# Kernel optimization log

Measured on AMD Instinct MI355X. Metric: run time of the kernel, lower is better.

## Reference

```python
import jax, jax.numpy as jnp
import numpy as np

BN_EPS = 1e-5

def conv1x1(x, w, b):
    # x: [N,C,T,V], w: [O,C], b: [O]
    return jnp.einsum('nctv,oc->notv', x, w) + b[None, :, None, None]

def conv9(x, w, b):
    # (9,1) temporal conv, padding (4,0). x: [N,C,T,V], w: [O,C,9], b: [O]
    out = jax.lax.conv_general_dilated(
        x, w[:, :, :, None], window_strides=(1, 1), padding=((4, 4), (0, 0)),
        dimension_numbers=('NCHW', 'OIHW', 'NCHW'))
    return out + b[None, :, None, None]

def attn_adj(f1, f2):
    # f1,f2: [N,inter,T,V] -> softmax over rows (axis -2) of [N,V,V]
    N, ic, T, V = f1.shape
    a1 = jnp.transpose(f1, (0, 3, 1, 2)).reshape(N, V, ic * T)  # permute(0,3,1,2).view
    a2 = f2.reshape(N, ic * T, V)
    scores = jnp.einsum('nvk,nkw->nvw', a1, a2) / (ic * T)
    return jax.nn.softmax(scores, axis=-2)


def setup_inputs() -> dict:
    key = jax.random.key(0)
    ks = jax.random.split(key, 16)
    N, C, T, V, S, IC = 16, 256, 64, 25, 3, 64
    s = lambda k, shape, sc=0.05: jax.random.normal(k, shape, dtype=jnp.float32) * sc
    return {
        'x': jax.random.normal(ks[0], (N, C, T, V), dtype=jnp.float32),
        'A': jax.random.uniform(ks[1], (S, V, V), dtype=jnp.float32),
        'PA': s(ks[2], (S, V, V), 1e-3),
        'wa': s(ks[3], (S, IC, C)), 'ba': jnp.zeros((S, IC), jnp.float32),
        'wb': s(ks[4], (S, IC, C)), 'bb': jnp.zeros((S, IC), jnp.float32),
        'wT1': s(ks[5], (S, IC, C, 9)), 'bT1': jnp.zeros((S, IC), jnp.float32),
        'wT2': s(ks[6], (S, IC, C, 9)), 'bT2': jnp.zeros((S, IC), jnp.float32),
        'wST11': s(ks[7], (S, IC, C, 9)), 'bST11': jnp.zeros((S, IC), jnp.float32),
        'wST12': s(ks[8], (S, IC, C, 9)), 'bST12': jnp.zeros((S, IC), jnp.float32),
        'wd': s(ks[9], (S, C, C)), 'bd': jnp.zeros((S, C), jnp.float32),
        'gamma': jnp.ones((C,), jnp.float32), 'beta': jnp.zeros((C,), jnp.float32),
        'bn_mean': jnp.zeros((C,), jnp.float32), 'bn_var': jnp.ones((C,), jnp.float32),
    }


def reference(x, A, PA, wa, ba, wb, bb, wT1, bT1, wT2, bT2,
              wST11, bST11, wST12, bST12, wd, bd, gamma, beta, bn_mean, bn_var):
    N, C, T, V = x.shape
    I = jnp.eye(V, dtype=x.dtype)
    # Chebyshev-like static graph transforms (computed once in __init__ in torch)
    A_ch4s = jax.nn.softmax((8 * A**4 - 4 * A**2 - 4 * A + I) / V, axis=-2)
    A_ch3 = 4 * A**2 - A - 2 * I
    A_all = A_ch3 + A_ch4s + PA  # [3,V,V]

    xf = x.reshape(N, C * T, V)
    y = 0.0
    for i in range(3):
        A1 = attn_adj(conv1x1(x, wa[i], ba[i]), conv1x1(x, wb[i], bb[i]))
        AT = attn_adj(conv9(x, wT1[i], bT1[i]), conv9(x, wT2[i], bT2[i]))
        # ModuleList append quirk: even i -> 1x1 conv (center tap), odd i -> (9,1) conv
        if i % 2 == 0:
            s1 = conv1x1(x, wST11[i, :, :, 4], bST11[i])
            s2 = conv1x1(x, wST12[i, :, :, 4], bST12[i])
        else:
            s1 = conv9(x, wST11[i], bST11[i])
            s2 = conv9(x, wST12[i], bST12[i])
        AST = attn_adj(s1, s2)
        Ai = A_all[i] + A1 + AT + AST  # [N,V,V]
        z = jnp.einsum('nkv,nvw->nkw', xf, Ai).reshape(N, C, T, V)
        y = y + conv1x1(z, wd[i], bd[i])

    yb = (y - bn_mean[None, :, None, None]) * (gamma[None, :, None, None]
         / jnp.sqrt(bn_var[None, :, None, None] + BN_EPS)) + beta[None, :, None, None]
    return jax.nn.relu(yb + x)  # down is identity (in_channels == out_channels)
```

## Files before the change

### kernel.cpp

```cpp
#include <hip/hip_runtime.h>
#include <hip/hip_bf16.h>

#define NN 16
#define CC 256
#define TT 64
#define VV 25
#define ICC 64
#define TV 1600
#define CTV 409600
#define NICTV 1638400

typedef __bf16 v8bf __attribute__((ext_vector_type(8)));
typedef __bf16 v4bf __attribute__((ext_vector_type(4)));
typedef float f32x16 __attribute__((ext_vector_type(16)));

struct ConvPairs {
  const __bf16* wA[5];
  const __bf16* wB[5];
  const float*  bA[5];
  const float*  bB[5];
};

__device__ __forceinline__ void gl_lds16(const __bf16* g, __bf16* l){
  __builtin_amdgcn_global_load_lds(
      (const __attribute__((address_space(1))) unsigned int*)g,
      (__attribute__((address_space(3))) unsigned int*)l, 16, 0, 0);
}

__global__ __launch_bounds__(256) void prep_k(
    const float* __restrict__ x, __bf16* __restrict__ xt,
    const float* __restrict__ wT1, const float* __restrict__ wT2,
    const float* __restrict__ wST11, const float* __restrict__ wST12,
    __bf16* __restrict__ wT1p, __bf16* __restrict__ wT2p,
    __bf16* __restrict__ wS1p, __bf16* __restrict__ wS2p,
    const float* __restrict__ wa, const float* __restrict__ wb,
    __bf16* __restrict__ wabp, __bf16* __restrict__ wScp,
    const float* __restrict__ wd, __bf16* __restrict__ wdb,
    const float* __restrict__ A, const float* __restrict__ PA,
    float* __restrict__ Aall, __bf16* __restrict__ zp){
  __shared__ __align__(16) float smf[64*65];
  __bf16* smb = (__bf16*)smf;
  int b = blockIdx.x;
  int tid = threadIdx.x;
  if (b < 64){
    int t = b >> 3, ch64 = (b >> 1) & 3, o2 = b & 1;
    const float* src; __bf16* dst;
    if (t < 3)      { src = wT1  + (size_t)t*147456;     dst = wT1p + (size_t)t*147456; }
    else if (t < 6) { src = wT2  + (size_t)(t-3)*147456; dst = wT2p + (size_t)(t-3)*147456; }
    else if (t == 6){ src = wST11 + 147456;              dst = wS1p; }
    else            { src = wST12 + 147456;              dst = wS2p; }
    const float* in = src + (size_t)(o2*32)*2304 + ch64*576;
    for (int i = tid; i < 32*576; i += 256){
      int row = i / 576, cc = i % 576;
      smb[i] = (__bf16)in[(size_t)row*2304 + cc];
    }
    __syncthreads();
    for (int i = tid; i < 18432; i += 256){
      int e = i & 7, l = (i >> 3) & 63, ks = (i >> 9) & 1;
      int r10 = i >> 10;
      int tap = r10 % 9, chh = r10 / 9;
      int ol = l & 31, hh = l >> 5;
      int cl = ks*16 + hh*8 + e;
      int c64 = chh*32 + cl;
      int ch8 = ch64*2 + chh;
      dst[(size_t)((((ch8*9 + tap)*2 + ks)*2 + o2)*512) + l*8 + e]
          = smb[ol*576 + c64*9 + tap];
    }
  } else if (b < 74){
    int u = b - 64;
    for (int it = 0; it < 8; ++it){
      int i = tid + it*256;
      int e = i & 7, l = (i >> 3) & 63, o2 = (i >> 9) & 1;
      int ks = (i >> 10) & 1, ch = i >> 11;
      int ol = l & 31, hh = l >> 5;
      int o = o2*32 + ol;
      int c = ch*32 + ks*16 + hh*8 + e;
      __bf16 v;
      if (u < 6){
        const float* w = (u < 3) ? (wa + (size_t)u*16384) : (wb + (size_t)(u-3)*16384);
        v = (__bf16)w[(size_t)o*256 + c];
      } else {
        int i9 = ((u == 6) || (u == 8)) ? 0 : 2;
        const float* w = ((u < 8) ? wST11 : wST12) + (size_t)i9*147456;
        v = (__bf16)w[((size_t)o*256 + c)*9 + 4];
      }
      __bf16* dst = (u < 6) ? (wabp + (size_t)u*16384) : (wScp + (size_t)(u-6)*16384);
      dst[i] = v;
    }
  } else if (b < 842){
    int i = (b-74)*256 + tid;
    if (i < 196608) wdb[i] = (__bf16)wd[i];
  } else if (b == 842){
    int t = tid;
    if (t < 75){
      int s = t / 25, w = t % 25;
      float a[25], m[25];
      float mx = -3.4e38f;
      for (int v = 0; v < 25; ++v){
        float av = A[(s*25 + v)*25 + w];
        a[v] = av;
        float d = (v == w) ? 1.f : 0.f;
        float mm = (8.f*av*av*av*av - 4.f*av*av - 4.f*av + d) * 0.04f;
        m[v] = mm;
        mx = fmaxf(mx, mm);
      }
      float sum = 0.f;
      for (int v = 0; v < 25; ++v){ float e = __expf(m[v]-mx); m[v] = e; sum += e; }
      float inv = 1.f/sum;
      for (int v = 0; v < 25; ++v){
        float av = a[v];
        float d = (v == w) ? 1.f : 0.f;
        Aall[(s*25+v)*25 + w] = m[v]*inv + 4.f*av*av - av - 2.f*d + PA[(s*25+v)*25+w];
      }
    } else if (t >= 128){
      zp[t-128] = (__bf16)0.f;
    }
  } else {
    int idx = b - 843;
    int p0 = (idx % 25)*64, c0 = ((idx/25) & 3)*64, n = idx/100;
    for (int i = tid; i < 4096; i += 256){
      int cc = i >> 6, pp = i & 63;
      smf[cc*65+pp] = x[(size_t)n*CTV + (size_t)(c0+cc)*TV + p0 + pp];
    }
    __syncthreads();
    for (int i = tid; i < 4096; i += 256){
      int pp = i >> 6, cc = i & 63;
      xt[((size_t)n*TV + p0+pp)*256 + c0+cc] = (__bf16)smf[cc*65+pp];
    }
  }
}

template<int NTAPS>
__global__ __launch_bounds__(512, 2) void conv11_k(const __bf16* __restrict__ xt,
    ConvPairs cp, const __bf16* __restrict__ zp, __bf16* __restrict__ fbuf){
  extern __shared__ __bf16 sm[];
  constexpr int HALO  = (NTAPS==9) ? 100 : 0;
  constexpr int NROWS = 512 + 2*HALO;
  constexpr int SLOTS = NROWS*4;
  constexpr int KSTG  = (SLOTS + 511)/512;
  constexpr int NSTEP = NTAPS*2;
  int p0 = blockIdx.x*512;
  int n  = blockIdx.y;
  int pr = blockIdx.z;
  int tid = threadIdx.x;
  int lane = tid & 63;
  int wave = tid >> 6;
  int which = wave >> 2, wq = wave & 3;
  int h = lane >> 5, l31 = lane & 31;
  const __bf16* wp = (which ? cp.wB[pr] : cp.wA[pr]) + lane*8;
  const __bf16* xtn = xt + (size_t)n*CTV;
  __bf16* buf0 = sm;
  __bf16* buf1 = sm + NROWS*32;

  f32x16 acc[2][4];
  #pragma unroll
  for (int a=0;a<2;++a)
    #pragma unroll
    for (int b=0;b<4;++b)
      #pragma unroll
      for (int r=0;r<16;++r) acc[a][b][r] = 0.f;

  int rowbase = wq*128 + l31;

  auto stage = [&](__bf16* bn, int ch){
    #pragma unroll
    for (int k=0; k<KSTG; ++k){
      int slot = k*512 + tid;
      if ((SLOTS & 511) && slot >= SLOTS) continue;
      int row = slot >> 2, g2 = slot & 3;
      int g = (g2 - row) & 3;
      int pg = p0 - HALO + row;
      const __bf16* src = ((unsigned)pg < 1600u)
          ? (xtn + (size_t)pg*256 + ch*32 + g*8) : (zp + g*8);
      gl_lds16(src, bn + (size_t)slot*8);
    }
  };
  auto ldA = [&](int ch, int s, v8bf* aa){
    int tap = s >> 1, ks = s & 1;
    size_t o = (size_t)(((ch*NTAPS + tap)*2 + ks)*2)*512;
    aa[0] = *(const v8bf*)(wp + o);
    aa[1] = *(const v8bf*)(wp + o + 512);
  };
  auto ldB = [&](const __bf16* bc, int s, v8bf* bb){
    int tap = s >> 1, ks = s & 1;
    int rowb = (NTAPS==9 ? tap*25 : 0) + rowbase;
    #pragma unroll
    for (int pq=0; pq<4; ++pq){
      int row = rowb + pq*32;
      int gs = ((ks*2 + h) + row) & 3;
      bb[pq] = *(const v8bf*)(bc + row*32 + gs*8);
    }
  };

  v8bf ar[2][2];
  ldA(0, 0, ar[0]);
  ldA(0, 1, ar[1]);
  stage(buf0, 0);
  __syncthreads();

  for (int ch=0; ch<8; ++ch){
    const __bf16* bc = (ch & 1) ? buf1 : buf0;
    __bf16*       bn = (ch & 1) ? buf0 : buf1;
    if (ch < 7) stage(bn, ch+1);
    v8bf bR[2][4];
    ldB(bc, 0, bR[0]);
    ldB(bc, 1, bR[1]);
    #pragma unroll
    for (int s=0; s<NSTEP; ++s){
      int c = s & 1;
      v8bf A0 = ar[c][0], A1 = ar[c][1];
      v8bf B0 = bR[c][0], B1 = bR[c][1], B2 = bR[c][2], B3 = bR[c][3];
      if (s+2 < NSTEP){
        ldB(bc, s+2, bR[c]);
        ldA(ch, s+2, ar[c]);
      } else if (ch < 7){
        ldA(ch+1, s+2-NSTEP, ar[c]);
      }
      acc[0][0] = __builtin_amdgcn_mfma_f32_32x32x16_bf16(A0, B0, acc[0][0], 0,0,0);
      acc[1][0] = __builtin_amdgcn_mfma_f32_32x32x16_bf16(A1, B0, acc[1][0], 0,0,0);
      acc[0][1] = __builtin_amdgcn_mfma_f32_32x32x16_bf16(A0, B1, acc[0][1], 0,0,0);
      acc[1][1] = __builtin_amdgcn_mfma_f32_32x32x16_bf16(A1, B1, acc[1][1], 0,0,0);
      acc[0][2] = __builtin_amdgcn_mfma_f32_32x32x16_bf16(A0, B2, acc[0][2], 0,0,0);
      acc[1][2] = __builtin_amdgcn_mfma_f32_32x32x16_bf16(A1, B2, acc[1][2], 0,0,0);
      acc[0][3] = __builtin_amdgcn_mfma_f32_32x32x16_bf16(A0, B3, acc[0][3], 0,0,0);
      acc[1][3] = __builtin_amdgcn_mfma_f32_32x32x16_bf16(A1, B3, acc[1][3], 0,0,0);
    }
    __syncthreads();
  }

  const float* bias = which ? cp.bB[pr] : cp.bA[pr];
  __bf16* outb = fbuf + (size_t)(pr*2 + which)*NICTV + (size_t)n*TV*64;
  #pragma unroll
  for (int pq=0; pq<4; ++pq){
    int p = p0 + wq*128 + pq*32 + l31;
    if (p >= 1600) continue;
    __bf16* orow = outb + (size_t)p*64;
    #pragma unroll
    for (int of=0; of<2; ++of){
      #pragma unroll
      for (int g=0; g<4; ++g){
        int og = of*32 + 8*g + 4*h;
        v4bf pk;
        #pragma unroll
        for (int j=0;j<4;++j) pk[j] = (__bf16)(acc[of][pq][4*g+j] + bias[og+j]);
        *(v4bf*)(orow + og) = pk;
      }
    }
  }
}

__global__ __launch_bounds__(256, 2) void ugemm5_k(const __bf16* __restrict__ xt,
    const __bf16* __restrict__ wdb, __bf16* __restrict__ ubuf){
  extern __shared__ __bf16 sm[];
  int p0 = blockIdx.x*128;
  int n  = blockIdx.y;
  int br = blockIdx.z;
  int tid = threadIdx.x;
  int lane = tid & 63;
  int os = tid >> 6;
  int h = lane >> 5, l31 = lane & 31;
  const __bf16* xtn = xt + (size_t)n*CTV;

  f32x16 acc[2][4];
  #pragma unroll
  for (int a=0;a<2;++a)
    #pragma unroll
    for (int b=0;b<4;++b)
      #pragma unroll
      for (int r=0;r<16;++r) acc[a][b][r] = 0.f;

  for (int s2 = tid; s2 < 128*32; s2 += 256){
    int row = s2 >> 5, g = s2 & 31;
    int pg = p0 + row;
    uint4 val = make_uint4(0u,0u,0u,0u);
    if (pg < 1600)
      val = *(const uint4*)(xtn + (size_t)pg*256 + g*8);
    int gs = (g + row) & 31;
    *(uint4*)(sm + row*256 + gs*8) = val;
  }
  __syncthreads();

  const __bf16* wl = wdb + ((size_t)br*256 + os*64 + l31)*256 + h*8;
  auto ldA = [&](int ks, v8bf& A0, v8bf& A1){
    A0 = *(const v8bf*)(wl + ks*16);
    A1 = *(const v8bf*)(wl + (size_t)32*256 + ks*16);
  };
  auto ldB = [&](int ks, v8bf* bb){
    #pragma unroll
    for (int pq=0; pq<4; ++pq){
      int row = pq*32 + l31;
      int gs = ((ks*2 + h) + row) & 31;
      bb[pq] = *(const v8bf*)(sm + row*256 + gs*8);
    }
  };
  v8bf a0[4], a1[4];
  ldA(0, a0[0], a1[0]);
  ldA(1, a0[1], a1[1]);
  ldA(2, a0[2], a1[2]);
  ldA(3, a0[3], a1[3]);
  v8bf bR[2][4];
  ldB(0, bR[0]);
  ldB(1, bR[1]);
  #pragma unroll
  for (int ks=0; ks<16; ++ks){
    int c2 = ks & 1, cur = ks & 3;
    v8bf B0 = bR[c2][0], B1 = bR[c2][1], B2 = bR[c2][2], B3 = bR[c2][3];
    v8bf A0 = a0[cur], A1 = a1[cur];
    if (ks+2 < 16) ldB(ks+2, bR[c2]);
    if (ks+4 < 16) ldA(ks+4, a0[cur], a1[cur]);
    acc[0][0] = __builtin_amdgcn_mfma_f32_32x32x16_bf16(A0, B0, acc[0][0], 0,0,0);
    acc[1][0] = __builtin_amdgcn_mfma_f32_32x32x16_bf16(A1, B0, acc[1][0], 0,0,0);
    acc[0][1] = __builtin_amdgcn_mfma_f32_32x32x16_bf16(A0, B1, acc[0][1], 0,0,0);
    acc[1][1] = __builtin_amdgcn_mfma_f32_32x32x16_bf16(A1, B1, acc[1][1], 0,0,0);
    acc[0][2] = __builtin_amdgcn_mfma_f32_32x32x16_bf16(A0, B2, acc[0][2], 0,0,0);
    acc[1][2] = __builtin_amdgcn_mfma_f32_32x32x16_bf16(A1, B2, acc[1][2], 0,0,0);
    acc[0][3] = __builtin_amdgcn_mfma_f32_32x32x16_bf16(A0, B3, acc[0][3], 0,0,0);
    acc[1][3] = __builtin_amdgcn_mfma_f32_32x32x16_bf16(A1, B3, acc[1][3], 0,0,0);
  }

  #pragma unroll
  for (int pq=0; pq<4; ++pq){
    int p = p0 + pq*32 + l31;
    if (p >= 1600) continue;
    __bf16* out = ubuf + ((size_t)(br*NN + n)*TV + p)*256;
    #pragma unroll
    for (int oq=0; oq<2; ++oq){
      #pragma unroll
      for (int g=0; g<4; ++g){
        int og = os*64 + oq*32 + 8*g + 4*h;
        v4bf pk;
        #pragma unroll
        for (int j=0;j<4;++j) pk[j] = (__bf16)acc[oq][pq][4*g+j];
        *(v4bf*)(out + og) = pk;
      }
    }
  }
}

__global__ __launch_bounds__(256) void scores_m_k(const __bf16* __restrict__ fbuf,
                                                  float* __restrict__ part, int pairbase){
  int n = blockIdx.y, pr = blockIdx.z;
  int tid = threadIdx.x;
  int lane = tid & 63;
  int wave = tid >> 6;
  int chunk = blockIdx.x*4 + wave;
  int h = lane >> 5, l31 = lane & 31;
  const __bf16* f1 = fbuf + (size_t)(pr*2)*NICTV   + (size_t)n*TV*64;
  const __bf16* f2 = fbuf + (size_t)(pr*2+1)*NICTV + (size_t)n*TV*64;
  int t0 = chunk*4;

  f32x16 acc;
  #pragma unroll
  for (int r=0;r<16;++r) acc[r] = 0.f;

  auto off = [&](int s)->size_t{
    int t = t0 + (s>>2), og = s&3;
    return ((size_t)(t*25 + l31))*64 + og*16 + h*8;
  };
  v8bf A[4], B[4];
  #pragma unroll
  for (int i=0; i<4; ++i){
    size_t o = off(i);
    A[i] = *(const v8bf*)(f1+o); B[i] = *(const v8bf*)(f2+o);
  }
  #pragma unroll
  for (int s=0; s<16; ++s){
    int cur = s & 3;
    v8bf Ac = A[cur], Bc = B[cur];
    if (s+4 < 16){
      size_t o2 = off(s+4);
      A[cur] = *(const v8bf*)(f1+o2);
      B[cur] = *(const v8bf*)(f2+o2);
    }
    acc = __builtin_amdgcn_mfma_f32_32x32x16_bf16(Ac, Bc, acc, 0,0,0);
  }

  size_t tile = (((size_t)(pairbase+pr)*NN + n)*16 + chunk);
  float* pt = part + tile*1024;
  #pragma unroll
  for (int r=0; r<16; ++r){
    int row = (r&3) + 8*(r>>2) + 4*h;
    pt[row*32 + l31] = acc[r];
  }
}

__global__ __launch_bounds__(64) void reduce_all_k(const float* __restrict__ part,
    const float* __restrict__ Aall, float* __restrict__ Ai3){
  const int pairbr[9] = {0,1,2,0,2, 0,1,2,1};
  int n = blockIdx.x, w = blockIdx.y;
  int lane = threadIdx.x;
  float accbr[3] = {0.f, 0.f, 0.f};
  for (int pr=0; pr<9; ++pr){
    float s = 0.f;
    if (lane < 25){
      const float* pp = part + (((size_t)pr*NN + n)*16)*1024 + lane*32 + w;
      #pragma unroll
      for (int ch=0; ch<16; ++ch) s += pp[(size_t)ch*1024];
    }
    s *= (1.f/4096.f);
    float mval = (lane<25) ? s : -3.4e38f;
    #pragma unroll
    for (int d=32; d>0; d>>=1) mval = fmaxf(mval, __shfl_xor(mval, d));
    float e = (lane<25) ? __expf(s - mval) : 0.f;
    float sum = e;
    #pragma unroll
    for (int d=32; d>0; d>>=1) sum += __shfl_xor(sum, d);
    accbr[pairbr[pr]] += e / sum;
  }
  if (lane < 25){
    #pragma unroll
    for (int br=0; br<3; ++br)
      Ai3[((size_t)br*NN + n)*625 + lane*25 + w] =
        Aall[br*625 + lane*25 + w] + accbr[br];
  }
}

__global__ __launch_bounds__(256) void yep_k(const float* __restrict__ x,
    const float* __restrict__ Ai3, const __bf16* __restrict__ ubuf,
    const float* __restrict__ bd, const float* __restrict__ gamma,
    const float* __restrict__ beta, const float* __restrict__ bnm,
    const float* __restrict__ bnv, float* __restrict__ out){
  __shared__ float ais[3][25*28];
  int t = blockIdx.x, n = blockIdx.y, o = threadIdx.x;
  for (int l=o; l<2100; l+=256){
    int br = l/700, r = l%700;
    int v = r/28, w = r%28;
    ais[br][v*28+w] = (w<25) ? Ai3[((size_t)br*NN + n)*625 + v*25 + w] : 0.f;
  }
  __syncthreads();
  float y[28];
  #pragma unroll
  for (int w=0;w<28;++w) y[w]=0.f;
  for (int br=0; br<3; ++br){
    const __bf16* up = ubuf + ((size_t)(br*NN + n)*TV + t*25)*256 + o;
    float uv[25];
    #pragma unroll
    for (int v=0;v<25;++v) uv[v] = (float)up[(size_t)v*256];
    const float* ab = ais[br];
    for (int v=0; v<25; ++v){
      float u = uv[v];
      #pragma unroll
      for (int j=0; j<7; ++j){
        float4 a4 = *(const float4*)(ab + v*28 + 4*j);
        y[4*j+0] = fmaf(u, a4.x, y[4*j+0]);
        y[4*j+1] = fmaf(u, a4.y, y[4*j+1]);
        y[4*j+2] = fmaf(u, a4.z, y[4*j+2]);
        y[4*j+3] = fmaf(u, a4.w, y[4*j+3]);
      }
    }
  }
  float bsum = bd[o] + bd[256+o] + bd[512+o];
  float sc = gamma[o] * rsqrtf(bnv[o] + 1e-5f);
  float m  = bnm[o], be = beta[o];
  const float* xr = x + (size_t)n*CTV + (size_t)o*TV + t*25;
  float* orow = out + (size_t)n*CTV + (size_t)o*TV + t*25;
  #pragma unroll
  for (int w=0; w<25; ++w)
    orow[w] = fmaxf((y[w] + bsum - m)*sc + be + xr[w], 0.f);
}

extern "C" void kernel_launch(void* const* d_in, const int* in_sizes, int n_in,
                              void* d_out, int out_size, void* d_ws, size_t ws_size,
                              hipStream_t stream) {
  const float* x     = (const float*)d_in[0];
  const float* A     = (const float*)d_in[1];
  const float* PA    = (const float*)d_in[2];
  const float* wa    = (const float*)d_in[3];
  const float* ba    = (const float*)d_in[4];
  const float* wb    = (const float*)d_in[5];
  const float* bb    = (const float*)d_in[6];
  const float* wT1   = (const float*)d_in[7];
  const float* bT1   = (const float*)d_in[8];
  const float* wT2   = (const float*)d_in[9];
  const float* bT2   = (const float*)d_in[10];
  const float* wST11 = (const float*)d_in[11];
  const float* bST11 = (const float*)d_in[12];
  const float* wST12 = (const float*)d_in[13];
  const float* bST12 = (const float*)d_in[14];
  const float* wd    = (const float*)d_in[15];
  const float* bd    = (const float*)d_in[16];
  const float* gamma = (const float*)d_in[17];
  const float* beta  = (const float*)d_in[18];
  const float* bnm   = (const float*)d_in[19];
  const float* bnv   = (const float*)d_in[20];

  char* W = (char*)d_ws;
  float*  Aall = (float*)W;  W += 8192;
  __bf16* zp   = (__bf16*)W; W += 256;
  float*  Ai3  = (float*)W;  W += 122880;
  __bf16* wabp = (__bf16*)W; W += 196608;
  __bf16* wScp = (__bf16*)W; W += 131072;
  __bf16* wT1p = (__bf16*)W; W += 884736;
  __bf16* wT2p = (__bf16*)W; W += 884736;
  __bf16* wS1p = (__bf16*)W; W += 294912;
  __bf16* wS2p = (__bf16*)W; W += 294912;
  __bf16* wdb  = (__bf16*)W; W += 393216;
  __bf16* xt   = (__bf16*)W; W += 13107200;
  char* R = W;               W += 39321600;
  float*  part = (float*)W;  W += 9437184;
  __bf16* fbuf = (__bf16*)R;
  __bf16* ubuf = (__bf16*)R;

  prep_k<<<2443, 256, 0, stream>>>(x, xt, wT1, wT2, wST11, wST12,
                                   wT1p, wT2p, wS1p, wS2p,
                                   wa, wb, wabp, wScp, wd, wdb, A, PA, Aall, zp);

  {
    ConvPairs cp;
    for (int i=0;i<3;++i){
      cp.wA[i] = wabp + (size_t)i*16384;      cp.wB[i] = wabp + (size_t)(3+i)*16384;
      cp.bA[i] = ba + i*64;                   cp.bB[i] = bb + i*64;
    }
    int evens[2] = {0, 2};
    for (int j=0;j<2;++j){
      int i = evens[j];
      cp.wA[3+j] = wScp + (size_t)j*16384;    cp.wB[3+j] = wScp + (size_t)(2+j)*16384;
      cp.bA[3+j] = bST11 + i*64;              cp.bB[3+j] = bST12 + i*64;
    }
    conv11_k<1><<<dim3(4,16,5), 512, 2*512*32*2, stream>>>(xt, cp, zp, fbuf);
    scores_m_k<<<dim3(4,16,5), 256, 0, stream>>>(fbuf, part, 0);
  }

  {
    ConvPairs cp;
    for (int i=0;i<3;++i){
      cp.wA[i] = wT1p + (size_t)i*147456;  cp.wB[i] = wT2p + (size_t)i*147456;
      cp.bA[i] = bT1 + i*64;               cp.bB[i] = bT2 + i*64;
    }
    cp.wA[3] = wS1p;  cp.wB[3] = wS2p;
    cp.bA[3] = bST11 + 64;  cp.bB[3] = bST12 + 64;
    cp.wA[4] = cp.wA[3]; cp.wB[4] = cp.wB[3]; cp.bA[4] = cp.bA[3]; cp.bB[4] = cp.bB[3];
    conv11_k<9><<<dim3(4,16,4), 512, 2*712*32*2, stream>>>(xt, cp, zp, fbuf);
    scores_m_k<<<dim3(4,16,4), 256, 0, stream>>>(fbuf, part, 5);
  }

  ugemm5_k<<<dim3(13,16,3), 256, 128*256*2, stream>>>(xt, wdb, ubuf);
  reduce_all_k<<<dim3(16,25), 64, 0, stream>>>(part, Aall, Ai3);
  yep_k<<<dim3(64,16), 256, 0, stream>>>(x, Ai3, ubuf, bd, gamma, beta, bnm, bnv,
                                         (float*)d_out);
}
```

Baseline: 353.2 us.

## Re-layout conv LDS staging and restructure ugemm to reuse x tile across branches

```diff
diff --git a/kernel.cpp b/kernel.cpp
--- a/kernel.cpp
+++ b/kernel.cpp
@@ -131,7 +131,7 @@
 }
 
 template<int NTAPS>
-__global__ __launch_bounds__(512, 2) void conv11_k(const __bf16* __restrict__ xt,
+__global__ __launch_bounds__(512, 2) void conv12_k(const __bf16* __restrict__ xt,
     ConvPairs cp, const __bf16* __restrict__ zp, __bf16* __restrict__ fbuf){
   extern __shared__ __bf16 sm[];
   constexpr int HALO  = (NTAPS==9) ? 100 : 0;
@@ -167,11 +167,20 @@
     for (int k=0; k<KSTG; ++k){
       int slot = k*512 + tid;
       if ((SLOTS & 511) && slot >= SLOTS) continue;
-      int row = slot >> 2, g2 = slot & 3;
-      int g = (g2 - row) & 3;
-      int pg = p0 - HALO + row;
-      const __bf16* src = ((unsigned)pg < 1600u)
-          ? (xtn + (size_t)pg*256 + ch*32 + g*8) : (zp + g*8);
+      const __bf16* src;
+      if (NTAPS == 1){
+        int l31s = slot & 31, f = slot >> 5;
+        int h_ = f & 1, ks_ = (f >> 1) & 1, pblk = f >> 2;
+        int pg = p0 + pblk*32 + l31s;
+        src = (pg < 1600) ? (xtn + (size_t)pg*256 + ch*32 + ks_*16 + h_*8)
+                          : zp;
+      } else {
+        int row = slot >> 2, g2 = slot & 3;
+        int g = (g2 - (row>>1)) & 3;
+        int pg = p0 - HALO + row;
+        src = ((unsigned)pg < 1600u) ? (xtn + (size_t)pg*256 + ch*32 + g*8)
+                                     : zp;
+      }
       gl_lds16(src, bn + (size_t)slot*8);
     }
   };
@@ -183,12 +192,16 @@
   };
   auto ldB = [&](const __bf16* bc, int s, v8bf* bb){
     int tap = s >> 1, ks = s & 1;
-    int rowb = (NTAPS==9 ? tap*25 : 0) + rowbase;
     #pragma unroll
     for (int pq=0; pq<4; ++pq){
-      int row = rowb + pq*32;
-      int gs = ((ks*2 + h) + row) & 3;
-      bb[pq] = *(const v8bf*)(bc + row*32 + gs*8);
+      if (NTAPS == 1){
+        int frag = ((wq*4 + pq)*2 + ks)*2 + h;
+        bb[pq] = *(const v8bf*)(bc + frag*256 + l31*8);
+      } else {
+        int row = tap*25 + rowbase + pq*32;
+        int gs = ((ks*2 + h) + (row>>1)) & 3;
+        bb[pq] = *(const v8bf*)(bc + row*32 + gs*8);
+      }
     }
   };
 
@@ -249,89 +262,83 @@
   }
 }
 
-__global__ __launch_bounds__(256, 2) void ugemm5_k(const __bf16* __restrict__ xt,
+__global__ __launch_bounds__(256, 2) void ugemm6_k(const __bf16* __restrict__ xt,
     const __bf16* __restrict__ wdb, __bf16* __restrict__ ubuf){
-  extern __shared__ __bf16 sm[];
-  int p0 = blockIdx.x*128;
+  __shared__ __bf16 sm[64*256];
+  int p0 = blockIdx.x*64;
   int n  = blockIdx.y;
-  int br = blockIdx.z;
   int tid = threadIdx.x;
   int lane = tid & 63;
   int os = tid >> 6;
   int h = lane >> 5, l31 = lane & 31;
   const __bf16* xtn = xt + (size_t)n*CTV;
 
-  f32x16 acc[2][4];
-  #pragma unroll
-  for (int a=0;a<2;++a)
-    #pragma unroll
-    for (int b=0;b<4;++b)
-      #pragma unroll
-      for (int r=0;r<16;++r) acc[a][b][r] = 0.f;
-
-  for (int s2 = tid; s2 < 128*32; s2 += 256){
+  for (int s2 = tid; s2 < 64*32; s2 += 256){
     int row = s2 >> 5, g = s2 & 31;
-    int pg = p0 + row;
-    uint4 val = make_uint4(0u,0u,0u,0u);
-    if (pg < 1600)
-      val = *(const uint4*)(xtn + (size_t)pg*256 + g*8);
+    uint4 val = *(const uint4*)(xtn + (size_t)(p0+row)*256 + g*8);
     int gs = (g + row) & 31;
     *(uint4*)(sm + row*256 + gs*8) = val;
   }
   __syncthreads();
 
-  const __bf16* wl = wdb + ((size_t)br*256 + os*64 + l31)*256 + h*8;
-  auto ldA = [&](int ks, v8bf& A0, v8bf& A1){
-    A0 = *(const v8bf*)(wl + ks*16);
-    A1 = *(const v8bf*)(wl + (size_t)32*256 + ks*16);
-  };
   auto ldB = [&](int ks, v8bf* bb){
     #pragma unroll
-    for (int pq=0; pq<4; ++pq){
+    for (int pq=0; pq<2; ++pq){
       int row = pq*32 + l31;
       int gs = ((ks*2 + h) + row) & 31;
       bb[pq] = *(const v8bf*)(sm + row*256 + gs*8);
     }
   };
-  v8bf a0[4], a1[4];
-  ldA(0, a0[0], a1[0]);
-  ldA(1, a0[1], a1[1]);
-  ldA(2, a0[2], a1[2]);
-  ldA(3, a0[3], a1[3]);
-  v8bf bR[2][4];
-  ldB(0, bR[0]);
-  ldB(1, bR[1]);
-  #pragma unroll
-  for (int ks=0; ks<16; ++ks){
-    int c2 = ks & 1, cur = ks & 3;
-    v8bf B0 = bR[c2][0], B1 = bR[c2][1], B2 = bR[c2][2], B3 = bR[c2][3];
-    v8bf A0 = a0[cur], A1 = a1[cur];
-    if (ks+2 < 16) ldB(ks+2, bR[c2]);
-    if (ks+4 < 16) ldA(ks+4, a0[cur], a1[cur]);
-    acc[0][0] = __builtin_amdgcn_mfma_f32_32x32x16_bf16(A0, B0, acc[0][0], 0,0,0);
-    acc[1][0] = __builtin_amdgcn_mfma_f32_32x32x16_bf16(A1, B0, acc[1][0], 0,0,0);
-    acc[0][1] = __builtin_amdgcn_mfma_f32_32x32x16_bf16(A0, B1, acc[0][1], 0,0,0);
-    acc[1][1] = __builtin_amdgcn_mfma_f32_32x32x16_bf16(A1, B1, acc[1][1], 0,0,0);
-    acc[0][2] = __builtin_amdgcn_mfma_f32_32x32x16_bf16(A0, B2, acc[0][2], 0,0,0);
-    acc[1][2] = __builtin_amdgcn_mfma_f32_32x32x16_bf16(A1, B2, acc[1][2], 0,0,0);
-    acc[0][3] = __builtin_amdgcn_mfma_f32_32x32x16_bf16(A0, B3, acc[0][3], 0,0,0);
-    acc[1][3] = __builtin_amdgcn_mfma_f32_32x32x16_bf16(A1, B3, acc[1][3], 0,0,0);
-  }
-
-  #pragma unroll
-  for (int pq=0; pq<4; ++pq){
-    int p = p0 + pq*32 + l31;
-    if (p >= 1600) continue;
-    __bf16* out = ubuf + ((size_t)(br*NN + n)*TV + p)*256;
-    #pragma unroll
-    for (int oq=0; oq<2; ++oq){
+
+  for (int br=0; br<3; ++br){
+    const __bf16* wl = wdb + ((size_t)br*256 + os*64 + l31)*256 + h*8;
+    auto ldA = [&](int ks, v8bf& A0, v8bf& A1){
+      A0 = *(const v8bf*)(wl + ks*16);
+      A1 = *(const v8bf*)(wl + (size_t)32*256 + ks*16);
+    };
+    f32x16 acc[2][2];
+    #pragma unroll
+    for (int a=0;a<2;++a)
       #pragma unroll
-      for (int g=0; g<4; ++g){
-        int og = os*64 + oq*32 + 8*g + 4*h;
-        v4bf pk;
+      for (int b=0;b<2;++b)
         #pragma unroll
-        for (int j=0;j<4;++j) pk[j] = (__bf16)acc[oq][pq][4*g+j];
-        *(v4bf*)(out + og) = pk;
+        for (int r=0;r<16;++r) acc[a][b][r] = 0.f;
+
+    v8bf a0[4], a1[4];
+    ldA(0, a0[0], a1[0]);
+    ldA(1, a0[1], a1[1]);
+    ldA(2, a0[2], a1[2]);
+    ldA(3, a0[3], a1[3]);
+    v8bf bR[2][2];
+    ldB(0, bR[0]);
+    ldB(1, bR[1]);
+    #pragma unroll
+    for (int ks=0; ks<16; ++ks){
+      int c2 = ks & 1, cur = ks & 3;
+      v8bf B0 = bR[c2][0], B1 = bR[c2][1];
+      v8bf A0 = a0[cur], A1 = a1[cur];
+      if (ks+2 < 16) ldB(ks+2, bR[c2]);
+      if (ks+4 < 16) ldA(ks+4, a0[cur], a1[cur]);
+      acc[0][0] = __builtin_amdgcn_mfma_f32_32x32x16_bf16(A0, B0, acc[0][0], 0,0,0);
+      acc[1][0] = __builtin_amdgcn_mfma_f32_32x32x16_bf16(A1, B0, acc[1][0], 0,0,0);
+      acc[0][1] = __builtin_amdgcn_mfma_f32_32x32x16_bf16(A0, B1, acc[0][1], 0,0,0);
+      acc[1][1] = __builtin_amdgcn_mfma_f32_32x32x16_bf16(A1, B1, acc[1][1], 0,0,0);
+    }
+
+    #pragma unroll
+    for (int pq=0; pq<2; ++pq){
+      int p = p0 + pq*32 + l31;
+      __bf16* out = ubuf + ((size_t)(br*NN + n)*TV + p)*256;
+      #pragma unroll
+      for (int oq=0; oq<2; ++oq){
+        #pragma unroll
+        for (int g=0; g<4; ++g){
+          int og = os*64 + oq*32 + 8*g + 4*h;
+          v4bf pk;
+          #pragma unroll
+          for (int j=0;j<4;++j) pk[j] = (__bf16)acc[oq][pq][4*g+j];
+          *(v4bf*)(out + og) = pk;
+        }
       }
     }
   }
@@ -517,7 +524,7 @@
       cp.wA[3+j] = wScp + (size_t)j*16384;    cp.wB[3+j] = wScp + (size_t)(2+j)*16384;
       cp.bA[3+j] = bST11 + i*64;              cp.bB[3+j] = bST12 + i*64;
     }
-    conv11_k<1><<<dim3(4,16,5), 512, 2*512*32*2, stream>>>(xt, cp, zp, fbuf);
+    conv12_k<1><<<dim3(4,16,5), 512, 2*512*32*2, stream>>>(xt, cp, zp, fbuf);
     scores_m_k<<<dim3(4,16,5), 256, 0, stream>>>(fbuf, part, 0);
   }
 
@@ -530,11 +537,11 @@
     cp.wA[3] = wS1p;  cp.wB[3] = wS2p;
     cp.bA[3] = bST11 + 64;  cp.bB[3] = bST12 + 64;
     cp.wA[4] = cp.wA[3]; cp.wB[4] = cp.wB[3]; cp.bA[4] = cp.bA[3]; cp.bB[4] = cp.bB[3];
-    conv11_k<9><<<dim3(4,16,4), 512, 2*712*32*2, stream>>>(xt, cp, zp, fbuf);
+    conv12_k<9><<<dim3(4,16,4), 512, 2*712*32*2, stream>>>(xt, cp, zp, fbuf);
     scores_m_k<<<dim3(4,16,4), 256, 0, stream>>>(fbuf, part, 5);
   }
 
-  ugemm5_k<<<dim3(13,16,3), 256, 128*256*2, stream>>>(xt, wdb, ubuf);
+  ugemm6_k<<<dim3(25,16), 256, 0, stream>>>(xt, wdb, ubuf);
   reduce_all_k<<<dim3(16,25), 64, 0, stream>>>(part, Aall, Ai3);
   yep_k<<<dim3(64,16), 256, 0, stream>>>(x, Ai3, ubuf, bd, gamma, beta, bnm, bnv,
                                          (float*)d_out);
```

Result: no change. 353.4 us (+0.1%).
